# Kernel optimization log

Hardware: AMD Instinct MI355X
Metric: run time of the kernel (lower is better)

Reference implementation:

```python
import jax, jax.numpy as jnp
import numpy as np

N_NODES = 100000
N_EDGES = 1600000
IN_DIM = 128
HIDDEN = 16
OUT_DIM = 40
QMAX = 255.0  # 2**8 - 1


def quant_dequant(x, noise):
    """Per-row uint8 stochastic quantize + dequantize (straight-through in bwd)."""
    rmin = jnp.min(x, axis=1)  # [N]
    rmax = jnp.max(x, axis=1)  # [N]
    rscale = QMAX / (rmax - rmin)  # [N]
    q = (x - rmin[:, None]) * rscale[:, None]
    q = jnp.clip(jnp.round(q + noise - 0.5), 0.0, QMAX)
    q = q.astype(jnp.uint8).astype(x.dtype)  # uint8 storage as in torch code
    dq = q / rscale[:, None] + rmin[:, None]
    # straight-through: original custom backward ignores quantization
    return x + jax.lax.stop_gradient(dq - x)


def spmm(row, col, vals, x, n_nodes):
    """z[i] = sum_{e: row[e]==i} vals[e] * x[col[e]]  (COO A @ x)."""
    gathered = vals[:, None] * x[col]  # [E, d]
    return jax.ops.segment_sum(gathered, row, num_segments=n_nodes)


def gcn_layer(x, W, noise, row, col, vals):
    dq = quant_dequant(x, noise)
    z = spmm(row, col, vals, dq, x.shape[0])
    return z @ W


def setup_inputs() -> dict:
    key = jax.random.key(0)
    ks = jax.random.split(key, 10)
    features = jax.random.normal(ks[0], (N_NODES, IN_DIM), dtype=jnp.float32)
    row = jax.random.randint(ks[1], (N_EDGES,), 0, N_NODES, dtype=jnp.int32)
    col = jax.random.randint(ks[2], (N_EDGES,), 0, N_NODES, dtype=jnp.int32)
    vals = jax.random.uniform(ks[3], (N_EDGES,), dtype=jnp.float32)
    W1 = jax.random.normal(ks[4], (IN_DIM, HIDDEN), dtype=jnp.float32) * (1.0 / np.sqrt(IN_DIM))
    W2 = jax.random.normal(ks[5], (HIDDEN, HIDDEN), dtype=jnp.float32) * (1.0 / np.sqrt(HIDDEN))
    W3 = jax.random.normal(ks[6], (HIDDEN, OUT_DIM), dtype=jnp.float32) * (1.0 / np.sqrt(HIDDEN))
    noise1 = jax.random.uniform(ks[7], (N_NODES, IN_DIM), dtype=jnp.float32)
    noise2 = jax.random.uniform(ks[8], (N_NODES, HIDDEN), dtype=jnp.float32)
    noise3 = jax.random.uniform(ks[9], (N_NODES, HIDDEN), dtype=jnp.float32)
    return {"features": features, "row": row, "col": col, "vals": vals,
            "W1": W1, "W2": W2, "W3": W3,
            "noise1": noise1, "noise2": noise2, "noise3": noise3}


def reference(features, row, col, vals, W1, W2, W3, noise1, noise2, noise3):
    h = jax.nn.relu(gcn_layer(features, W1, noise1, row, col, vals))
    h = jax.nn.relu(gcn_layer(h, W2, noise2, row, col, vals))
    out = gcn_layer(h, W3, noise3, row, col, vals)
    return out
```

## Files before the change

### kernel.cpp

```cpp
#include <hip/hip_runtime.h>
#include <hip/hip_fp16.h>

#define N_NODES 100000
#define N_EDGES 1600000
#define IN_DIM 128
#define HIDDEN 16
#define OUT_DIM 40
#define QMAXF 255.0f

#define NB 512
#define RPB 196
#define NB_USED 511
#define BUCKET_CAP 4096
#define TILE 4096
#define EPT 16
#define NBLK_BIN ((N_EDGES + TILE - 1) / TILE)
#define HALF_CAP 2560

typedef float vfloat4 __attribute__((ext_vector_type(4)));

__device__ __forceinline__ float qd_one(float x, float noise, float rmin,
                                        float rscale, float inv) {
    float q = rintf((x - rmin) * rscale + noise - 0.5f);
    q = fminf(fmaxf(q, 0.0f), QMAXF);
    return q * inv + rmin;
}


__global__ __launch_bounds__(512) void k_initcur(int* __restrict__ cursor) {
    const int i = threadIdx.x;
    if (i < NB) cursor[i] = i * BUCKET_CAP;
}

__global__ __launch_bounds__(256) void k_bin(
    const int* __restrict__ row, const int* __restrict__ col,
    const float* __restrict__ vals, int* __restrict__ cursor,
    long long* __restrict__ es) {
    __shared__ int hist[NB];
    __shared__ int psum[256];
    __shared__ int lofs[NB];
    __shared__ int lcur[NB];
    __shared__ int gbase[NB];
    __shared__ long long stage[TILE];
    __shared__ int dsti[TILE];

    const int tid = threadIdx.x;
    for (int i = tid; i < NB; i += 256) hist[i] = 0;
    __syncthreads();

    int bk[EPT];
    long long ev[EPT];
    const int e0 = blockIdx.x * TILE;
#pragma unroll
    for (int k = 0; k < EPT; ++k) {
        const int e = e0 + k * 256 + tid;
        if (e < N_EDGES) {
            const int r = __builtin_nontemporal_load(row + e);
            const int cc = __builtin_nontemporal_load(col + e);
            const float vv = __builtin_nontemporal_load(vals + e);
            const int b = r / RPB;
            bk[k] = b;
            const unsigned lo = (unsigned)(cc | ((r - b * RPB) << 17));
            ev[k] = (long long)(((unsigned long long)__float_as_uint(vv) << 32) |
                                lo);
            atomicAdd(&hist[b], 1);
        } else {
            bk[k] = -1;
        }
    }
    __syncthreads();

    const int h0 = hist[2 * tid], h1 = hist[2 * tid + 1];
    psum[tid] = h0 + h1;
    __syncthreads();
    for (int off = 1; off < 256; off <<= 1) {
        int x = (tid >= off) ? psum[tid - off] : 0;
        __syncthreads();
        psum[tid] += x;
        __syncthreads();
    }
    const int excl = (tid == 0) ? 0 : psum[tid - 1];
    lofs[2 * tid] = excl;
    lofs[2 * tid + 1] = excl + h0;
    lcur[2 * tid] = excl;
    lcur[2 * tid + 1] = excl + h0;
    if (h0) gbase[2 * tid] = atomicAdd(&cursor[2 * tid], h0);
    if (h1) gbase[2 * tid + 1] = atomicAdd(&cursor[2 * tid + 1], h1);
    __syncthreads();

#pragma unroll
    for (int k = 0; k < EPT; ++k) {
        if (bk[k] >= 0) {
            const int b = bk[k];
            const int lp = atomicAdd(&lcur[b], 1);
            stage[lp] = ev[k];
            dsti[lp] = gbase[b] + (lp - lofs[b]);
        }
    }
    __syncthreads();

    const int S = psum[255];
    for (int i = tid; i < S; i += 256)
        __builtin_nontemporal_store(stage[i], es + dsti[i]);
}

__global__ __launch_bounds__(256) void k_sort(
    const int* __restrict__ cursor, long long* __restrict__ es,
    int* __restrict__ rowEnd) {
    __shared__ int hist[256];
    __shared__ int psum[256];
    __shared__ int cur[256];
    __shared__ long long stage[BUCKET_CAP];

    const int b = blockIdx.x;
    const int tid = threadIdx.x;
    const int start = b * BUCKET_CAP;
    const int cnt = cursor[b] - start;

    hist[tid] = 0;
    __syncthreads();

    long long ev[EPT];
    int rr[EPT];
#pragma unroll
    for (int k = 0; k < EPT; ++k) {
        const int i = k * 256 + tid;
        if (i < cnt) {
            ev[k] = es[start + i];
            rr[k] = (int)(((unsigned)ev[k]) >> 17);
            atomicAdd(&hist[rr[k]], 1);
        } else {
            rr[k] = -1;
        }
    }
    __syncthreads();

    psum[tid] = hist[tid];
    __syncthreads();
    for (int off = 1; off < 256; off <<= 1) {
        int x = (tid >= off) ? psum[tid - off] : 0;
        __syncthreads();
        psum[tid] += x;
        __syncthreads();
    }
    if (tid < RPB) rowEnd[b * RPB + tid] = start + psum[tid];
    cur[tid] = psum[tid] - hist[tid];
    __syncthreads();

#pragma unroll
    for (int k = 0; k < EPT; ++k) {
        if (rr[k] >= 0) {
            const int pos = atomicAdd(&cur[rr[k]], 1);
            stage[pos] = ev[k];
        }
    }
    __syncthreads();

    for (int i = tid; i < cnt; i += 256)
        __builtin_nontemporal_store(stage[i], es + start + i);
}

__global__ __launch_bounds__(256) void k_spmm3(
    const int* __restrict__ rowEnd, const long long* __restrict__ es,
    const __half* __restrict__ y, float* __restrict__ z) {
    __shared__ long long stage[HALF_CAP];
    __shared__ int rp[100];

    const int b = blockIdx.x >> 1;
    const int hb = blockIdx.x & 1;
    const int tid = threadIdx.x;
    const int r0 = hb * 98;
    const int gb = b * RPB;
    const int bstart = b * BUCKET_CAP;

    __shared__ int sh_se[2];
    if (tid == 0) {
        sh_se[0] = (r0 == 0) ? bstart : rowEnd[gb + r0 - 1];
        sh_se[1] = rowEnd[gb + r0 + 97];
    }
    if (tid < 99) {
        rp[tid + 1] = rowEnd[gb + r0 + tid];
    }
    __syncthreads();
    const int estart = sh_se[0];
    const int cnt = sh_se[1] - estart;
    if (tid == 0) rp[0] = estart;
    __syncthreads();

    for (int i = tid; i < cnt; i += 256)
        stage[i] = __builtin_nontemporal_load(es + estart + i);
    __syncthreads();

    if (tid >= 196) return;
    const int lr = tid >> 1;
    const int h = tid & 1;
    const int grow = gb + r0 + lr;
    int j = rp[lr] - estart;
    const int je = rp[lr + 1] - estart;

    float acc[8];
#pragma unroll
    for (int i = 0; i < 8; ++i) acc[i] = 0.0f;

    for (; j + 4 <= je; j += 4) {
        const long long e0 = stage[j], e1 = stage[j + 1];
        const long long e2 = stage[j + 2], e3 = stage[j + 3];
        const uint4 a0 = *(const uint4*)(y + (size_t)(((unsigned)e0) & 0x1FFFF) * HIDDEN + h * 8);
        const uint4 a1 = *(const uint4*)(y + (size_t)(((unsigned)e1) & 0x1FFFF) * HIDDEN + h * 8);
        const uint4 a2 = *(const uint4*)(y + (size_t)(((unsigned)e2) & 0x1FFFF) * HIDDEN + h * 8);
        const uint4 a3 = *(const uint4*)(y + (size_t)(((unsigned)e3) & 0x1FFFF) * HIDDEN + h * 8);
        const float v0 = __uint_as_float((unsigned)((unsigned long long)e0 >> 32));
        const float v1 = __uint_as_float((unsigned)((unsigned long long)e1 >> 32));
        const float v2 = __uint_as_float((unsigned)((unsigned long long)e2 >> 32));
        const float v3 = __uint_as_float((unsigned)((unsigned long long)e3 >> 32));
        const unsigned* p0 = (const unsigned*)&a0;
        const unsigned* p1 = (const unsigned*)&a1;
        const unsigned* p2 = (const unsigned*)&a2;
        const unsigned* p3 = (const unsigned*)&a3;
#pragma unroll
        for (int q = 0; q < 4; ++q) {
            float2 f;
            f = __half22float2(*(const __half2*)&p0[q]);
            acc[2 * q] += v0 * f.x; acc[2 * q + 1] += v0 * f.y;
            f = __half22float2(*(const __half2*)&p1[q]);
            acc[2 * q] += v1 * f.x; acc[2 * q + 1] += v1 * f.y;
            f = __half22float2(*(const __half2*)&p2[q]);
            acc[2 * q] += v2 * f.x; acc[2 * q + 1] += v2 * f.y;
            f = __half22float2(*(const __half2*)&p3[q]);
            acc[2 * q] += v3 * f.x; acc[2 * q + 1] += v3 * f.y;
        }
    }
    for (; j < je; ++j) {
        const long long e = stage[j];
        const float v = __uint_as_float((unsigned)((unsigned long long)e >> 32));
        const uint4 a = *(const uint4*)(y + (size_t)(((unsigned)e) & 0x1FFFF) * HIDDEN + h * 8);
        const unsigned* p = (const unsigned*)&a;
#pragma unroll
        for (int q = 0; q < 4; ++q) {
            const float2 f = __half22float2(*(const __half2*)&p[q]);
            acc[2 * q] += v * f.x;
            acc[2 * q + 1] += v * f.y;
        }
    }

    if (grow < N_NODES) {
        vfloat4* zr = (vfloat4*)(z + (size_t)grow * HIDDEN + h * 8);
        __builtin_nontemporal_store(*(const vfloat4*)&acc[0], zr);
        __builtin_nontemporal_store(*(const vfloat4*)&acc[4], zr + 1);
    }
}


__global__ __launch_bounds__(256) void k_qd_gemm1(
    const float* __restrict__ feat, const float* __restrict__ noise,
    const float* __restrict__ W1, __half* __restrict__ y) {
    __shared__ float dqbuf[4][IN_DIM];
    const int lane = threadIdx.x & 63;
    const int wv = threadIdx.x >> 6;
    const int col = lane & 15;
    const int kg = lane >> 4;

    float w1r[32];
#pragma unroll
    for (int i = 0; i < 32; ++i) w1r[i] = W1[(kg * 32 + i) * HIDDEN + col];

    const int ngroups = N_NODES / 4;
    for (int g = blockIdx.x; g < ngroups; g += gridDim.x) {
        const int node = g * 4 + wv;
        const unsigned long long xr = __builtin_nontemporal_load(
            (const unsigned long long*)(feat + (size_t)node * IN_DIM) + lane);
        const unsigned long long nr = __builtin_nontemporal_load(
            (const unsigned long long*)(noise + (size_t)node * IN_DIM) + lane);
        const float xx = __uint_as_float((unsigned)xr);
        const float xy = __uint_as_float((unsigned)(xr >> 32));
        const float nx = __uint_as_float((unsigned)nr);
        const float ny = __uint_as_float((unsigned)(nr >> 32));
        float m = fminf(xx, xy), M = fmaxf(xx, xy);
#pragma unroll
        for (int off = 1; off < 64; off <<= 1) {
            m = fminf(m, __shfl_xor(m, off));
            M = fmaxf(M, __shfl_xor(M, off));
        }
        const float rscale = QMAXF / (M - m);
        const float inv = (M - m) / QMAXF;
        float2 dq;
        dq.x = qd_one(xx, nx, m, rscale, inv);
        dq.y = qd_one(xy, ny, m, rscale, inv);
        ((float2*)dqbuf[wv])[lane] = dq;
        __syncthreads();
        float acc = 0.0f;
        const float* dqk = dqbuf[wv] + kg * 32;
#pragma unroll
        for (int i = 0; i < 32; ++i) acc += dqk[i] * w1r[i];
        acc += __shfl_xor(acc, 16);
        acc += __shfl_xor(acc, 32);
        if (lane < 16) y[(size_t)node * HIDDEN + lane] = __float2half(acc);
        __syncthreads();
    }
}

__global__ __launch_bounds__(256) void k_qd_gemm16(
    const float* __restrict__ zin, const float* __restrict__ noise,
    const float* __restrict__ W2, __half* __restrict__ y) {
    __shared__ float w[HIDDEN * HIDDEN];
    w[threadIdx.x] = W2[threadIdx.x];
    __syncthreads();
    const int t = blockIdx.x * 256 + threadIdx.x;
    if (t >= N_NODES) return;
    float x[16], nz[16];
    {
        const float4* zr = (const float4*)(zin + (size_t)t * HIDDEN);
        const float4* nr = (const float4*)(noise + (size_t)t * HIDDEN);
#pragma unroll
        for (int i = 0; i < 4; ++i) {
            ((float4*)x)[i] = zr[i];
            ((float4*)nz)[i] = nr[i];
        }
    }
#pragma unroll
    for (int i = 0; i < 16; ++i) x[i] = fmaxf(x[i], 0.0f);
    float m = x[0], M = x[0];
#pragma unroll
    for (int i = 1; i < 16; ++i) { m = fminf(m, x[i]); M = fmaxf(M, x[i]); }
    const float rscale = QMAXF / (M - m);
    const float inv = (M - m) / QMAXF;
    float acc[16];
#pragma unroll
    for (int j = 0; j < 16; ++j) acc[j] = 0.0f;
#pragma unroll
    for (int k = 0; k < 16; ++k) {
        const float d = qd_one(x[k], nz[k], m, rscale, inv);
        const float4* wr = (const float4*)(w + k * 16);
#pragma unroll
        for (int j4 = 0; j4 < 4; ++j4) {
            float4 ww = wr[j4];
            acc[4 * j4 + 0] += d * ww.x;
            acc[4 * j4 + 1] += d * ww.y;
            acc[4 * j4 + 2] += d * ww.z;
            acc[4 * j4 + 3] += d * ww.w;
        }
    }
    __half hb[16];
#pragma unroll
    for (int i = 0; i < 16; ++i) hb[i] = __float2half(acc[i]);
    float4* yr = (float4*)(y + (size_t)t * HIDDEN);
    yr[0] = ((float4*)hb)[0];
    yr[1] = ((float4*)hb)[1];
}

__global__ __launch_bounds__(256) void k_qd16(
    const float* __restrict__ zin, const float* __restrict__ noise,
    __half* __restrict__ y) {
    const int t = blockIdx.x * 256 + threadIdx.x;
    if (t >= N_NODES) return;
    float x[16], nz[16];
    {
        const float4* zr = (const float4*)(zin + (size_t)t * HIDDEN);
        const float4* nr = (const float4*)(noise + (size_t)t * HIDDEN);
#pragma unroll
        for (int i = 0; i < 4; ++i) {
            ((float4*)x)[i] = zr[i];
            ((float4*)nz)[i] = nr[i];
        }
    }
#pragma unroll
    for (int i = 0; i < 16; ++i) x[i] = fmaxf(x[i], 0.0f);
    float m = x[0], M = x[0];
#pragma unroll
    for (int i = 1; i < 16; ++i) { m = fminf(m, x[i]); M = fmaxf(M, x[i]); }
    const float rscale = QMAXF / (M - m);
    const float inv = (M - m) / QMAXF;
    __half hb[16];
#pragma unroll
    for (int i = 0; i < 16; ++i)
        hb[i] = __float2half(qd_one(x[i], nz[i], m, rscale, inv));
    float4* yr = (float4*)(y + (size_t)t * HIDDEN);
    yr[0] = ((float4*)hb)[0];
    yr[1] = ((float4*)hb)[1];
}

__global__ __launch_bounds__(256) void k_gemm_out(
    const float* __restrict__ z, const float* __restrict__ W3,
    float* __restrict__ out) {
    __shared__ float w[HIDDEN * OUT_DIM];
    for (int i = threadIdx.x; i < HIDDEN * OUT_DIM; i += 256) w[i] = W3[i];
    __syncthreads();
    const int t = blockIdx.x * 256 + threadIdx.x;
    if (t >= N_NODES) return;
    float x[16];
    {
        const float4* zr = (const float4*)(z + (size_t)t * HIDDEN);
#pragma unroll
        for (int i = 0; i < 4; ++i) ((float4*)x)[i] = zr[i];
    }
    float acc[OUT_DIM];
#pragma unroll
    for (int j = 0; j < OUT_DIM; ++j) acc[j] = 0.0f;
#pragma unroll
    for (int k = 0; k < 16; ++k) {
        const float d = x[k];
        const float4* wr = (const float4*)(w + k * OUT_DIM);
#pragma unroll
        for (int j4 = 0; j4 < OUT_DIM / 4; ++j4) {
            float4 ww = wr[j4];
            acc[4 * j4 + 0] += d * ww.x;
            acc[4 * j4 + 1] += d * ww.y;
            acc[4 * j4 + 2] += d * ww.z;
            acc[4 * j4 + 3] += d * ww.w;
        }
    }
    float4* orow = (float4*)(out + (size_t)t * OUT_DIM);
#pragma unroll
    for (int i = 0; i < OUT_DIM / 4; ++i) orow[i] = ((float4*)acc)[i];
}

extern "C" void kernel_launch(void* const* d_in, const int* in_sizes, int n_in,
                              void* d_out, int out_size, void* d_ws,
                              size_t ws_size, hipStream_t stream) {
    const float* feat = (const float*)d_in[0];
    const int* row = (const int*)d_in[1];
    const int* col = (const int*)d_in[2];
    const float* vals = (const float*)d_in[3];
    const float* W1 = (const float*)d_in[4];
    const float* W2 = (const float*)d_in[5];
    const float* W3 = (const float*)d_in[6];
    const float* n1 = (const float*)d_in[7];
    const float* n2 = (const float*)d_in[8];
    const float* n3 = (const float*)d_in[9];
    float* out = (float*)d_out;

    __half* yh = (__half*)d_ws;
    float* z = (float*)(yh + (size_t)N_NODES * HIDDEN);
    int* cursor = (int*)(z + (size_t)N_NODES * HIDDEN);
    int* rowEnd = cursor + NB;
    long long* es = (long long*)(rowEnd + NB * RPB);

    const int nodeBlocks = (N_NODES + 255) / 256;

    k_initcur<<<1, 512, 0, stream>>>(cursor);
    k_bin<<<NBLK_BIN, 256, 0, stream>>>(row, col, vals, cursor, es);
    k_sort<<<NB_USED, 256, 0, stream>>>(cursor, es, rowEnd);

    k_qd_gemm1<<<2500, 256, 0, stream>>>(feat, n1, W1, yh);
    k_spmm3<<<NB_USED * 2, 256, 0, stream>>>(rowEnd, es, yh, z);

    k_qd_gemm16<<<nodeBlocks, 256, 0, stream>>>(z, n2, W2, yh);
    k_spmm3<<<NB_USED * 2, 256, 0, stream>>>(rowEnd, es, yh, z);

    k_qd16<<<nodeBlocks, 256, 0, stream>>>(z, n3, yh);
    k_spmm3<<<NB_USED * 2, 256, 0, stream>>>(rowEnd, es, yh, z);
    k_gemm_out<<<nodeBlocks, 256, 0, stream>>>(z, W3, out);
}
```

Baseline: 281.4 us.

## Fuse node-wise quant/GEMM epilogues into SpMM and merge sort with layer-1 GEMM

Each SpMM kernel now applies ReLU, per-row quant-dequant and the small dense GEMM in its epilogue, with the two threads that share a row exchanging halves through shuffles. This removes the fp32 z round-trips and the separate per-node kernels. The bucket sort and the first-layer quantize+GEMM now run as different block ranges of a single launch so they can overlap. The cursor initialisation is replaced by a memset with relative offsets. The cost is higher register and LDS use in the fused kernels, which may lower occupancy.

```diff
diff --git a/kernel.cpp b/kernel.cpp
--- a/kernel.cpp
+++ b/kernel.cpp
@@ -16,6 +16,7 @@
 #define EPT 16
 #define NBLK_BIN ((N_EDGES + TILE - 1) / TILE)
 #define HALF_CAP 2560
+#define GEMM1_BLOCKS 2500
 
 typedef float vfloat4 __attribute__((ext_vector_type(4)));
 
@@ -26,11 +27,6 @@
     return q * inv + rmin;
 }
 
-
-__global__ __launch_bounds__(512) void k_initcur(int* __restrict__ cursor) {
-    const int i = threadIdx.x;
-    if (i < NB) cursor[i] = i * BUCKET_CAP;
-}
 
 __global__ __launch_bounds__(256) void k_bin(
     const int* __restrict__ row, const int* __restrict__ col,
@@ -84,8 +80,11 @@
     lofs[2 * tid + 1] = excl + h0;
     lcur[2 * tid] = excl;
     lcur[2 * tid + 1] = excl + h0;
-    if (h0) gbase[2 * tid] = atomicAdd(&cursor[2 * tid], h0);
-    if (h1) gbase[2 * tid + 1] = atomicAdd(&cursor[2 * tid + 1], h1);
+    if (h0)
+        gbase[2 * tid] = 2 * tid * BUCKET_CAP + atomicAdd(&cursor[2 * tid], h0);
+    if (h1)
+        gbase[2 * tid + 1] =
+            (2 * tid + 1) * BUCKET_CAP + atomicAdd(&cursor[2 * tid + 1], h1);
     __syncthreads();
 
 #pragma unroll
@@ -104,82 +103,151 @@
         __builtin_nontemporal_store(stage[i], es + dsti[i]);
 }
 
-__global__ __launch_bounds__(256) void k_sort(
+
+struct SortLds {
+    long long stage[BUCKET_CAP];
+    int hist[256];
+    int psum[256];
+    int cur[256];
+};
+union K1Lds {
+    SortLds s;
+    float dqbuf[4][IN_DIM];
+};
+
+__global__ __launch_bounds__(256, 4) void k_sort_gemm1(
     const int* __restrict__ cursor, long long* __restrict__ es,
-    int* __restrict__ rowEnd) {
-    __shared__ int hist[256];
-    __shared__ int psum[256];
-    __shared__ int cur[256];
-    __shared__ long long stage[BUCKET_CAP];
-
-    const int b = blockIdx.x;
+    int* __restrict__ rowEnd, const float* __restrict__ feat,
+    const float* __restrict__ noise, const float* __restrict__ W1,
+    __half* __restrict__ y) {
+    __shared__ K1Lds u;
     const int tid = threadIdx.x;
-    const int start = b * BUCKET_CAP;
-    const int cnt = cursor[b] - start;
-
-    hist[tid] = 0;
-    __syncthreads();
-
-    long long ev[EPT];
-    int rr[EPT];
-#pragma unroll
-    for (int k = 0; k < EPT; ++k) {
-        const int i = k * 256 + tid;
-        if (i < cnt) {
-            ev[k] = es[start + i];
-            rr[k] = (int)(((unsigned)ev[k]) >> 17);
-            atomicAdd(&hist[rr[k]], 1);
-        } else {
-            rr[k] = -1;
-        }
-    }
-    __syncthreads();
-
-    psum[tid] = hist[tid];
-    __syncthreads();
-    for (int off = 1; off < 256; off <<= 1) {
-        int x = (tid >= off) ? psum[tid - off] : 0;
-        __syncthreads();
-        psum[tid] += x;
-        __syncthreads();
-    }
-    if (tid < RPB) rowEnd[b * RPB + tid] = start + psum[tid];
-    cur[tid] = psum[tid] - hist[tid];
-    __syncthreads();
-
-#pragma unroll
-    for (int k = 0; k < EPT; ++k) {
-        if (rr[k] >= 0) {
-            const int pos = atomicAdd(&cur[rr[k]], 1);
-            stage[pos] = ev[k];
-        }
-    }
-    __syncthreads();
-
-    for (int i = tid; i < cnt; i += 256)
-        __builtin_nontemporal_store(stage[i], es + start + i);
+
+    if (blockIdx.x < NB_USED) {
+        const int b = blockIdx.x;
+        const int start = b * BUCKET_CAP;
+        const int cnt = cursor[b];
+
+        u.s.hist[tid] = 0;
+        __syncthreads();
+
+        long long ev[EPT];
+        int rr[EPT];
+#pragma unroll
+        for (int k = 0; k < EPT; ++k) {
+            const int i = k * 256 + tid;
+            if (i < cnt) {
+                ev[k] = es[start + i];
+                rr[k] = (int)(((unsigned)ev[k]) >> 17);
+                atomicAdd(&u.s.hist[rr[k]], 1);
+            } else {
+                rr[k] = -1;
+            }
+        }
+        __syncthreads();
+
+        u.s.psum[tid] = u.s.hist[tid];
+        __syncthreads();
+        for (int off = 1; off < 256; off <<= 1) {
+            int x = (tid >= off) ? u.s.psum[tid - off] : 0;
+            __syncthreads();
+            u.s.psum[tid] += x;
+            __syncthreads();
+        }
+        if (tid < RPB) rowEnd[b * RPB + tid] = start + u.s.psum[tid];
+        u.s.cur[tid] = u.s.psum[tid] - u.s.hist[tid];
+        __syncthreads();
+
+#pragma unroll
+        for (int k = 0; k < EPT; ++k) {
+            if (rr[k] >= 0) {
+                const int pos = atomicAdd(&u.s.cur[rr[k]], 1);
+                u.s.stage[pos] = ev[k];
+            }
+        }
+        __syncthreads();
+
+        for (int i = tid; i < cnt; i += 256)
+            __builtin_nontemporal_store(u.s.stage[i], es + start + i);
+    } else {
+        const int vb = blockIdx.x - NB_USED;
+        const int lane = tid & 63;
+        const int wv = tid >> 6;
+        const int col = lane & 15;
+        const int kg = lane >> 4;
+
+        float w1r[32];
+#pragma unroll
+        for (int i = 0; i < 32; ++i) w1r[i] = W1[(kg * 32 + i) * HIDDEN + col];
+
+        const int ngroups = N_NODES / 4;
+        for (int g = vb; g < ngroups; g += GEMM1_BLOCKS) {
+            const int node = g * 4 + wv;
+            const unsigned long long xr = __builtin_nontemporal_load(
+                (const unsigned long long*)(feat + (size_t)node * IN_DIM) +
+                lane);
+            const unsigned long long nr = __builtin_nontemporal_load(
+                (const unsigned long long*)(noise + (size_t)node * IN_DIM) +
+                lane);
+            const float xx = __uint_as_float((unsigned)xr);
+            const float xy = __uint_as_float((unsigned)(xr >> 32));
+            const float nx = __uint_as_float((unsigned)nr);
+            const float ny = __uint_as_float((unsigned)(nr >> 32));
+            float m = fminf(xx, xy), M = fmaxf(xx, xy);
+#pragma unroll
+            for (int off = 1; off < 64; off <<= 1) {
+                m = fminf(m, __shfl_xor(m, off));
+                M = fmaxf(M, __shfl_xor(M, off));
+            }
+            const float rscale = QMAXF / (M - m);
+            const float inv = (M - m) / QMAXF;
+            float2 dq;
+            dq.x = qd_one(xx, nx, m, rscale, inv);
+            dq.y = qd_one(xy, ny, m, rscale, inv);
+            ((float2*)u.dqbuf[wv])[lane] = dq;
+            __syncthreads();
+            float acc = 0.0f;
+            const float* dqk = u.dqbuf[wv] + kg * 32;
+#pragma unroll
+            for (int i = 0; i < 32; ++i) acc += dqk[i] * w1r[i];
+            acc += __shfl_xor(acc, 16);
+            acc += __shfl_xor(acc, 32);
+            if (lane < 16) y[(size_t)node * HIDDEN + lane] = __float2half(acc);
+            __syncthreads();
+        }
+    }
 }
 
-__global__ __launch_bounds__(256) void k_spmm3(
+
+template <int LAYER>
+__global__ __launch_bounds__(256, 4) void k_spmm_f(
     const int* __restrict__ rowEnd, const long long* __restrict__ es,
-    const __half* __restrict__ y, float* __restrict__ z) {
+    const __half* __restrict__ y, const float* __restrict__ noise,
+    const float* __restrict__ W, __half* __restrict__ yout,
+    float* __restrict__ out) {
     __shared__ long long stage[HALF_CAP];
     __shared__ int rp[100];
+    __shared__ int sh_se[2];
+    __shared__ float wsh[LAYER == 1 ? (HIDDEN * HIDDEN)
+                                    : (LAYER == 3 ? (HIDDEN * OUT_DIM) : 4)];
 
     const int b = blockIdx.x >> 1;
-    const int hb = blockIdx.x & 1;
+    const int hbk = blockIdx.x & 1;
     const int tid = threadIdx.x;
-    const int r0 = hb * 98;
+    const int r0 = hbk * 98;
     const int gb = b * RPB;
     const int bstart = b * BUCKET_CAP;
 
-    __shared__ int sh_se[2];
     if (tid == 0) {
         sh_se[0] = (r0 == 0) ? bstart : rowEnd[gb + r0 - 1];
         sh_se[1] = rowEnd[gb + r0 + 97];
     }
-    if (tid < 99) {
-        rp[tid + 1] = rowEnd[gb + r0 + tid];
+    if (tid < 99) rp[tid + 1] = rowEnd[gb + r0 + tid];
+    if (LAYER == 1) {
+        wsh[tid] = W[tid];
+    }
+    if (LAYER == 3) {
+        for (int i = tid; i < HIDDEN * OUT_DIM; i += 256) wsh[i] = W[i];
     }
     __syncthreads();
     const int estart = sh_se[0];
@@ -243,175 +311,88 @@
         }
     }
 
-    if (grow < N_NODES) {
-        vfloat4* zr = (vfloat4*)(z + (size_t)grow * HIDDEN + h * 8);
-        __builtin_nontemporal_store(*(const vfloat4*)&acc[0], zr);
-        __builtin_nontemporal_store(*(const vfloat4*)&acc[4], zr + 1);
-    }
-}
-
-
-__global__ __launch_bounds__(256) void k_qd_gemm1(
-    const float* __restrict__ feat, const float* __restrict__ noise,
-    const float* __restrict__ W1, __half* __restrict__ y) {
-    __shared__ float dqbuf[4][IN_DIM];
-    const int lane = threadIdx.x & 63;
-    const int wv = threadIdx.x >> 6;
-    const int col = lane & 15;
-    const int kg = lane >> 4;
-
-    float w1r[32];
-#pragma unroll
-    for (int i = 0; i < 32; ++i) w1r[i] = W1[(kg * 32 + i) * HIDDEN + col];
-
-    const int ngroups = N_NODES / 4;
-    for (int g = blockIdx.x; g < ngroups; g += gridDim.x) {
-        const int node = g * 4 + wv;
-        const unsigned long long xr = __builtin_nontemporal_load(
-            (const unsigned long long*)(feat + (size_t)node * IN_DIM) + lane);
-        const unsigned long long nr = __builtin_nontemporal_load(
-            (const unsigned long long*)(noise + (size_t)node * IN_DIM) + lane);
-        const float xx = __uint_as_float((unsigned)xr);
-        const float xy = __uint_as_float((unsigned)(xr >> 32));
-        const float nx = __uint_as_float((unsigned)nr);
-        const float ny = __uint_as_float((unsigned)(nr >> 32));
-        float m = fminf(xx, xy), M = fmaxf(xx, xy);
-#pragma unroll
-        for (int off = 1; off < 64; off <<= 1) {
-            m = fminf(m, __shfl_xor(m, off));
-            M = fmaxf(M, __shfl_xor(M, off));
-        }
+    if (grow >= N_NODES) return;
+
+    if (LAYER == 1 || LAYER == 2) {
+#pragma unroll
+        for (int i = 0; i < 8; ++i) acc[i] = fmaxf(acc[i], 0.0f);
+        float m = acc[0], M = acc[0];
+#pragma unroll
+        for (int i = 1; i < 8; ++i) {
+            m = fminf(m, acc[i]);
+            M = fmaxf(M, acc[i]);
+        }
+        m = fminf(m, __shfl_xor(m, 1));
+        M = fmaxf(M, __shfl_xor(M, 1));
         const float rscale = QMAXF / (M - m);
         const float inv = (M - m) / QMAXF;
-        float2 dq;
-        dq.x = qd_one(xx, nx, m, rscale, inv);
-        dq.y = qd_one(xy, ny, m, rscale, inv);
-        ((float2*)dqbuf[wv])[lane] = dq;
-        __syncthreads();
-        float acc = 0.0f;
-        const float* dqk = dqbuf[wv] + kg * 32;
-#pragma unroll
-        for (int i = 0; i < 32; ++i) acc += dqk[i] * w1r[i];
-        acc += __shfl_xor(acc, 16);
-        acc += __shfl_xor(acc, 32);
-        if (lane < 16) y[(size_t)node * HIDDEN + lane] = __float2half(acc);
-        __syncthreads();
-    }
-}
-
-__global__ __launch_bounds__(256) void k_qd_gemm16(
-    const float* __restrict__ zin, const float* __restrict__ noise,
-    const float* __restrict__ W2, __half* __restrict__ y) {
-    __shared__ float w[HIDDEN * HIDDEN];
-    w[threadIdx.x] = W2[threadIdx.x];
-    __syncthreads();
-    const int t = blockIdx.x * 256 + threadIdx.x;
-    if (t >= N_NODES) return;
-    float x[16], nz[16];
-    {
-        const float4* zr = (const float4*)(zin + (size_t)t * HIDDEN);
-        const float4* nr = (const float4*)(noise + (size_t)t * HIDDEN);
-#pragma unroll
-        for (int i = 0; i < 4; ++i) {
-            ((float4*)x)[i] = zr[i];
-            ((float4*)nz)[i] = nr[i];
-        }
-    }
-#pragma unroll
-    for (int i = 0; i < 16; ++i) x[i] = fmaxf(x[i], 0.0f);
-    float m = x[0], M = x[0];
-#pragma unroll
-    for (int i = 1; i < 16; ++i) { m = fminf(m, x[i]); M = fmaxf(M, x[i]); }
-    const float rscale = QMAXF / (M - m);
-    const float inv = (M - m) / QMAXF;
-    float acc[16];
-#pragma unroll
-    for (int j = 0; j < 16; ++j) acc[j] = 0.0f;
-#pragma unroll
-    for (int k = 0; k < 16; ++k) {
-        const float d = qd_one(x[k], nz[k], m, rscale, inv);
-        const float4* wr = (const float4*)(w + k * 16);
-#pragma unroll
-        for (int j4 = 0; j4 < 4; ++j4) {
-            float4 ww = wr[j4];
-            acc[4 * j4 + 0] += d * ww.x;
-            acc[4 * j4 + 1] += d * ww.y;
-            acc[4 * j4 + 2] += d * ww.z;
-            acc[4 * j4 + 3] += d * ww.w;
-        }
-    }
-    __half hb[16];
-#pragma unroll
-    for (int i = 0; i < 16; ++i) hb[i] = __float2half(acc[i]);
-    float4* yr = (float4*)(y + (size_t)t * HIDDEN);
-    yr[0] = ((float4*)hb)[0];
-    yr[1] = ((float4*)hb)[1];
-}
-
-__global__ __launch_bounds__(256) void k_qd16(
-    const float* __restrict__ zin, const float* __restrict__ noise,
-    __half* __restrict__ y) {
-    const int t = blockIdx.x * 256 + threadIdx.x;
-    if (t >= N_NODES) return;
-    float x[16], nz[16];
-    {
-        const float4* zr = (const float4*)(zin + (size_t)t * HIDDEN);
-        const float4* nr = (const float4*)(noise + (size_t)t * HIDDEN);
-#pragma unroll
-        for (int i = 0; i < 4; ++i) {
-            ((float4*)x)[i] = zr[i];
-            ((float4*)nz)[i] = nr[i];
-        }
-    }
-#pragma unroll
-    for (int i = 0; i < 16; ++i) x[i] = fmaxf(x[i], 0.0f);
-    float m = x[0], M = x[0];
-#pragma unroll
-    for (int i = 1; i < 16; ++i) { m = fminf(m, x[i]); M = fmaxf(M, x[i]); }
-    const float rscale = QMAXF / (M - m);
-    const float inv = (M - m) / QMAXF;
-    __half hb[16];
-#pragma unroll
-    for (int i = 0; i < 16; ++i)
-        hb[i] = __float2half(qd_one(x[i], nz[i], m, rscale, inv));
-    float4* yr = (float4*)(y + (size_t)t * HIDDEN);
-    yr[0] = ((float4*)hb)[0];
-    yr[1] = ((float4*)hb)[1];
-}
-
-__global__ __launch_bounds__(256) void k_gemm_out(
-    const float* __restrict__ z, const float* __restrict__ W3,
-    float* __restrict__ out) {
-    __shared__ float w[HIDDEN * OUT_DIM];
-    for (int i = threadIdx.x; i < HIDDEN * OUT_DIM; i += 256) w[i] = W3[i];
-    __syncthreads();
-    const int t = blockIdx.x * 256 + threadIdx.x;
-    if (t >= N_NODES) return;
-    float x[16];
-    {
-        const float4* zr = (const float4*)(z + (size_t)t * HIDDEN);
-#pragma unroll
-        for (int i = 0; i < 4; ++i) ((float4*)x)[i] = zr[i];
-    }
-    float acc[OUT_DIM];
-#pragma unroll
-    for (int j = 0; j < OUT_DIM; ++j) acc[j] = 0.0f;
-#pragma unroll
-    for (int k = 0; k < 16; ++k) {
-        const float d = x[k];
-        const float4* wr = (const float4*)(w + k * OUT_DIM);
-#pragma unroll
-        for (int j4 = 0; j4 < OUT_DIM / 4; ++j4) {
-            float4 ww = wr[j4];
-            acc[4 * j4 + 0] += d * ww.x;
-            acc[4 * j4 + 1] += d * ww.y;
-            acc[4 * j4 + 2] += d * ww.z;
-            acc[4 * j4 + 3] += d * ww.w;
-        }
-    }
-    float4* orow = (float4*)(out + (size_t)t * OUT_DIM);
-#pragma unroll
-    for (int i = 0; i < OUT_DIM / 4; ++i) orow[i] = ((float4*)acc)[i];
+        float nz[8];
+        {
+            const float4* nr =
+                (const float4*)(noise + (size_t)grow * HIDDEN + h * 8);
+            ((float4*)nz)[0] = nr[0];
+            ((float4*)nz)[1] = nr[1];
+        }
+        float dq[8];
+#pragma unroll
+        for (int i = 0; i < 8; ++i)
+            dq[i] = qd_one(acc[i], nz[i], m, rscale, inv);
+
+        if (LAYER == 2) {
+            __half hb8[8];
+#pragma unroll
+            for (int i = 0; i < 8; ++i) hb8[i] = __float2half(dq[i]);
+            *(float4*)(yout + (size_t)grow * HIDDEN + h * 8) = *(float4*)hb8;
+        } else {
+            float dp[8];
+#pragma unroll
+            for (int i = 0; i < 8; ++i) dp[i] = __shfl_xor(dq[i], 1);
+            const int kb = h * 8;
+            const int pb = 8 - kb;
+            const float* wmy = wsh + kb * HIDDEN + kb;
+            const float* wpr = wsh + pb * HIDDEN + kb;
+            float o[8];
+#pragma unroll
+            for (int jj = 0; jj < 8; ++jj) o[jj] = 0.0f;
+#pragma unroll
+            for (int i = 0; i < 8; ++i) {
+#pragma unroll
+                for (int jj = 0; jj < 8; ++jj) {
+                    o[jj] += dq[i] * wmy[i * HIDDEN + jj];
+                    o[jj] += dp[i] * wpr[i * HIDDEN + jj];
+                }
+            }
+            __half hb8[8];
+#pragma unroll
+            for (int jj = 0; jj < 8; ++jj) hb8[jj] = __float2half(o[jj]);
+            *(float4*)(yout + (size_t)grow * HIDDEN + kb) = *(float4*)hb8;
+        }
+    } else {
+        float ap[8];
+#pragma unroll
+        for (int i = 0; i < 8; ++i) ap[i] = __shfl_xor(acc[i], 1);
+        const int kb = h * 8;
+        const int pb = 8 - kb;
+        const int ob = h * 20;
+        const float* wmy = wsh + kb * OUT_DIM + ob;
+        const float* wpr = wsh + pb * OUT_DIM + ob;
+        float o[20];
+#pragma unroll
+        for (int jj = 0; jj < 20; ++jj) o[jj] = 0.0f;
+#pragma unroll
+        for (int i = 0; i < 8; ++i) {
+#pragma unroll
+            for (int jj = 0; jj < 20; ++jj) {
+                o[jj] += acc[i] * wmy[i * OUT_DIM + jj];
+                o[jj] += ap[i] * wpr[i * OUT_DIM + jj];
+            }
+        }
+        float* orow = out + (size_t)grow * OUT_DIM + ob;
+#pragma unroll
+        for (int j4 = 0; j4 < 5; ++j4)
+            __builtin_nontemporal_store(((const vfloat4*)o)[j4],
+                                        (vfloat4*)orow + j4);
+    }
 }
 
 extern "C" void kernel_launch(void* const* d_in, const int* in_sizes, int n_in,
@@ -429,25 +410,21 @@
     const float* n3 = (const float*)d_in[9];
     float* out = (float*)d_out;
 
-    __half* yh = (__half*)d_ws;
-    float* z = (float*)(yh + (size_t)N_NODES * HIDDEN);
-    int* cursor = (int*)(z + (size_t)N_NODES * HIDDEN);
+    __half* yh1 = (__half*)d_ws;
+    __half* yh2 = yh1 + (size_t)N_NODES * HIDDEN;
+    int* cursor = (int*)(yh2 + (size_t)N_NODES * HIDDEN);
     int* rowEnd = cursor + NB;
     long long* es = (long long*)(rowEnd + NB * RPB);
 
-    const int nodeBlocks = (N_NODES + 255) / 256;
-
-    k_initcur<<<1, 512, 0, stream>>>(cursor);
+    hipMemsetAsync(cursor, 0, NB * sizeof(int), stream);
     k_bin<<<NBLK_BIN, 256, 0, stream>>>(row, col, vals, cursor, es);
-    k_sort<<<NB_USED, 256, 0, stream>>>(cursor, es, rowEnd);
-
-    k_qd_gemm1<<<2500, 256, 0, stream>>>(feat, n1, W1, yh);
-    k_spmm3<<<NB_USED * 2, 256, 0, stream>>>(rowEnd, es, yh, z);
-
-    k_qd_gemm16<<<nodeBlocks, 256, 0, stream>>>(z, n2, W2, yh);
-    k_spmm3<<<NB_USED * 2, 256, 0, stream>>>(rowEnd, es, yh, z);
-
-    k_qd16<<<nodeBlocks, 256, 0, stream>>>(z, n3, yh);
-    k_spmm3<<<NB_USED * 2, 256, 0, stream>>>(rowEnd, es, yh, z);
-    k_gemm_out<<<nodeBlocks, 256, 0, stream>>>(z, W3, out);
+    k_sort_gemm1<<<NB_USED + GEMM1_BLOCKS, 256, 0, stream>>>(
+        cursor, es, rowEnd, feat, n1, W1, yh1);
+
+    k_spmm_f<1><<<NB_USED * 2, 256, 0, stream>>>(rowEnd, es, yh1, n2, W2, yh2,
+                                                 nullptr);
+    k_spmm_f<2><<<NB_USED * 2, 256, 0, stream>>>(rowEnd, es, yh2, n3, nullptr,
+                                                 yh1, nullptr);
+    k_spmm_f<3><<<NB_USED * 2, 256, 0, stream>>>(rowEnd, es, yh1, nullptr, W3,
+                                                 nullptr, out);
 }
```

After: 275.0 us. 2.3% less time.
